# Optimization experiments

Hardware: AMD Instinct MI355X
Metric: run time of the kernel (lower is better)

The kernel has to match this reference:

```python
import jax, jax.numpy as jnp
import numpy as np
from functools import partial

C = 256
N_HEADS = 8
OFFSET_RANGE = 2.0


def _dwconv(x, w):
    # depthwise conv, SAME padding; w: (C,1,k,k)
    c = x.shape[1]
    return jax.lax.conv_general_dilated(
        x, w, window_strides=(1, 1), padding='SAME',
        feature_group_count=c, dimension_numbers=('NCHW', 'OIHW', 'NCHW'))


def _grid_sample_bilinear(x, gx, gy):
    # x: (B,C,H,W); gx,gy: (B,H,W) normalized in [-1,1]; align_corners=True
    B, Cc, H, W = x.shape
    ix = (gx + 1.0) * 0.5 * (W - 1)
    iy = (gy + 1.0) * 0.5 * (H - 1)
    x0f = jnp.floor(ix)
    y0f = jnp.floor(iy)
    fx = (ix - x0f)[:, None, :, :].reshape(B, 1, H * W)
    fy = (iy - y0f)[:, None, :, :].reshape(B, 1, H * W)
    x0 = jnp.clip(x0f.astype(jnp.int32), 0, W - 1)
    x1 = jnp.clip(x0 + 1, 0, W - 1)
    y0 = jnp.clip(y0f.astype(jnp.int32), 0, H - 1)
    y1 = jnp.clip(y0 + 1, 0, H - 1)
    xf = x.reshape(B, Cc, H * W)

    def gather(yi, xi):
        idx = (yi * W + xi).reshape(B, H * W)
        return jax.vmap(lambda f, i: f[:, i])(xf, idx)  # (B,C,N)

    v00 = gather(y0, x0)
    v01 = gather(y0, x1)
    v10 = gather(y1, x0)
    v11 = gather(y1, x1)
    out = (v00 * (1 - fx) * (1 - fy) + v01 * fx * (1 - fy)
           + v10 * (1 - fx) * fy + v11 * fx * fy)
    return out.reshape(B, Cc, H, W)


def setup_inputs() -> dict:
    key = jax.random.key(0)
    ks = jax.random.split(key, 11)
    B, H, W = 1, 64, 64
    s = 0.05
    return {
        'x': jax.random.normal(ks[0], (B, C, H, W), jnp.float32),
        'offset_weights': jnp.ones((3,), jnp.float32) + 0.1 * jax.random.normal(ks[1], (3,)),
        'w3': s * jax.random.normal(ks[2], (C, 1, 3, 3), jnp.float32),
        'w5': s * jax.random.normal(ks[3], (C, 1, 5, 5), jnp.float32),
        'w7': s * jax.random.normal(ks[4], (C, 1, 7, 7), jnp.float32),
        'w_offproj': s * jax.random.normal(ks[5], (2, C), jnp.float32),
        'wq': s * jax.random.normal(ks[6], (C, C), jnp.float32),
        'wk': s * jax.random.normal(ks[7], (C, C), jnp.float32),
        'wv': s * jax.random.normal(ks[8], (C, C), jnp.float32),
        'wo': s * jax.random.normal(ks[9], (C, C), jnp.float32),
        'beta': jnp.asarray(0.5, jnp.float32),
    }


def reference(x, offset_weights, w3, w5, w7, w_offproj, wq, wk, wv, wo, beta):
    B, Cc, H, W = x.shape
    head_dim = Cc // N_HEADS
    scale = head_dim ** -0.5
    N = H * W

    # multi-scale depthwise offset features
    off_feat = (_dwconv(x, w3) * offset_weights[0]
                + _dwconv(x, w5) * offset_weights[1]
                + _dwconv(x, w7) * offset_weights[2])
    offset = jnp.einsum('oc,bchw->bohw', w_offproj, jax.nn.relu(off_feat))  # (B,2,H,W) = (y,x)

    # reference points: ((i+0.5)/(size-1))*2 - 1
    ref_y = ((jnp.arange(H, dtype=jnp.float32) + 0.5) / (H - 1.0)) * 2.0 - 1.0
    ref_x = ((jnp.arange(W, dtype=jnp.float32) + 0.5) / (W - 1.0)) * 2.0 - 1.0
    gy = jnp.clip(ref_y[None, :, None] + jnp.tanh(offset[:, 0]) * OFFSET_RANGE, -1.0, 1.0)
    gx = jnp.clip(ref_x[None, None, :] + jnp.tanh(offset[:, 1]) * OFFSET_RANGE, -1.0, 1.0)
    x_sampled = _grid_sample_bilinear(x, gx, gy)

    # Manhattan decay bias
    yy = jnp.repeat(jnp.arange(H), W)
    xx = jnp.tile(jnp.arange(W), H)
    dist = (jnp.abs(yy[:, None] - yy[None, :]) + jnp.abs(xx[:, None] - xx[None, :])).astype(jnp.float32)
    decay = jnp.exp(-dist / (jnp.abs(beta) + 1e-6))  # (N,N)

    q = jnp.einsum('oc,bchw->bohw', wq, x).reshape(B, N_HEADS, head_dim, N)
    k = jnp.einsum('oc,bchw->bohw', wk, x_sampled).reshape(B, N_HEADS, head_dim, N)
    v = jnp.einsum('oc,bchw->bohw', wv, x_sampled).reshape(B, N_HEADS, head_dim, N)

    attn = jnp.einsum('bhdn,bhdm->bhnm', q, k) * scale + decay[None, None]
    attn = jax.nn.softmax(attn, axis=-1)
    out = jnp.einsum('bhnm,bhdm->bhdn', attn, v).reshape(B, Cc, H, W)
    return jnp.einsum('oc,bchw->bohw', wo, out)
```

## Files before the change

kernel.cpp:

```cpp
#include <hip/hip_runtime.h>
#include <hip/hip_bf16.h>


typedef __bf16 bf16x8 __attribute__((ext_vector_type(8)));
typedef float f32x4 __attribute__((ext_vector_type(4)));

__device__ __forceinline__ f32x4 mfma16(bf16x8 a, bf16x8 b, f32x4 c) {
    return __builtin_amdgcn_mfma_f32_16x16x32_bf16(a, b, c, 0, 0, 0);
}

__device__ __forceinline__ unsigned pack_bf16(float pa, float pb) {
    return __builtin_amdgcn_perm(__float_as_uint(pb), __float_as_uint(pa), 0x07060302u);
}

__global__ void transpose_kernel(const float* __restrict__ x,
                                 float* __restrict__ xTf,
                                 __hip_bfloat16* __restrict__ xTb) {
    __shared__ float tile[32][33];
    const int p0 = blockIdx.x * 32, c0 = blockIdx.y * 32;
    const int tx = threadIdx.x, ty = threadIdx.y;
#pragma unroll
    for (int i = 0; i < 4; ++i)
        tile[ty + i * 8][tx] = x[(size_t)(c0 + ty + i * 8) * 4096 + p0 + tx];
    __syncthreads();
#pragma unroll
    for (int i = 0; i < 4; ++i) {
        const float v = tile[tx][ty + i * 8];
        const size_t o = (size_t)(p0 + ty + i * 8) * 256 + c0 + tx;
        xTf[o] = v;
        xTb[o] = __float2bfloat16(v);
    }
}

__global__ void prep_kernel(const float* __restrict__ w3, const float* __restrict__ w5,
                            const float* __restrict__ w7, const float* __restrict__ ow,
                            const float* __restrict__ wq, const float* __restrict__ wk,
                            const float* __restrict__ wv, const float* __restrict__ wo,
                            float* __restrict__ wcomb, __hip_bfloat16* __restrict__ wb) {
    const int b = blockIdx.x;
    if (b < 49) {
        const int i = b, c = threadIdx.x;
        const int dy = i / 7, dx = i % 7;
        float val = ow[2] * w7[c * 49 + i];
        if (dy >= 1 && dy <= 5 && dx >= 1 && dx <= 5)
            val += ow[1] * w5[c * 25 + (dy - 1) * 5 + (dx - 1)];
        if (dy >= 2 && dy <= 4 && dx >= 2 && dx <= 4)
            val += ow[0] * w3[c * 9 + (dy - 2) * 3 + (dx - 2)];
        wcomb[i * 256 + c] = val;
    } else {
        const int idx = (b - 49) * 256 + threadIdx.x;
        const int m = idx >> 16;
        const float* src = (m == 0) ? wq : (m == 1) ? wk : (m == 2) ? wv : wo;
        const float sc = (m == 0) ? 0.25507535f : 1.0f;
        wb[idx] = __float2bfloat16(src[idx & 65535] * sc);
    }
}

__global__ __launch_bounds__(256) void sample_kernel(
    const float* __restrict__ xTf, const float* __restrict__ wcomb,
    const float* __restrict__ wop, __hip_bfloat16* __restrict__ xsT) {
    const int b = blockIdx.x;
    const int y = b >> 3;
    const int x0 = (b & 7) * 8;
    const int c = threadIdx.x;

    float wc[49];
#pragma unroll
    for (int i = 0; i < 49; ++i) wc[i] = wcomb[i * 256 + c];

    float acc[8];
#pragma unroll
    for (int px = 0; px < 8; ++px) acc[px] = 0.f;

#pragma unroll
    for (int dy = 0; dy < 7; ++dy) {
        const int yy = y + dy - 3;
        if (yy < 0 || yy > 63) continue;
        float v[14];
#pragma unroll
        for (int j = 0; j < 14; ++j) {
            const int xx = x0 - 3 + j;
            v[j] = (xx >= 0 && xx <= 63) ? xTf[(size_t)(yy * 64 + xx) * 256 + c] : 0.f;
        }
#pragma unroll
        for (int px = 0; px < 8; ++px)
#pragma unroll
            for (int dx = 0; dx < 7; ++dx)
                acc[px] = fmaf(v[px + dx], wc[dy * 7 + dx], acc[px]);
    }

    const float wy = wop[c], wx = wop[256 + c];
    float s[16];
#pragma unroll
    for (int px = 0; px < 8; ++px) {
        const float r = fmaxf(acc[px], 0.f);
        s[px] = wy * r;
        s[8 + px] = wx * r;
    }
#pragma unroll
    for (int off = 1; off < 64; off <<= 1)
#pragma unroll
        for (int i = 0; i < 16; ++i) s[i] += __shfl_xor(s[i], off, 64);

    __shared__ float red[4][16];
    const int lane = c & 63, wid = c >> 6;
    if (lane == 0)
#pragma unroll
        for (int i = 0; i < 16; ++i) red[wid][i] = s[i];
    __syncthreads();

#pragma unroll
    for (int px = 0; px < 8; ++px) {
        const float offy = red[0][px] + red[1][px] + red[2][px] + red[3][px];
        const float offx = red[0][8 + px] + red[1][8 + px] + red[2][8 + px] + red[3][8 + px];
        const int pxa = x0 + px;
        const float refy = ((y + 0.5f) / 63.0f) * 2.0f - 1.0f;
        const float refx = ((pxa + 0.5f) / 63.0f) * 2.0f - 1.0f;
        const float gy = fminf(fmaxf(refy + tanhf(offy) * 2.0f, -1.0f), 1.0f);
        const float gx = fminf(fmaxf(refx + tanhf(offx) * 2.0f, -1.0f), 1.0f);
        const float iy = (gy + 1.0f) * 31.5f;
        const float ix = (gx + 1.0f) * 31.5f;
        const float y0f = floorf(iy), x0f = floorf(ix);
        const float fy = iy - y0f, fx = ix - x0f;
        int yi0 = min(max((int)y0f, 0), 63), xi0 = min(max((int)x0f, 0), 63);
        int yi1 = min(yi0 + 1, 63), xi1 = min(xi0 + 1, 63);
        const float v00 = xTf[(size_t)(yi0 * 64 + xi0) * 256 + c];
        const float v01 = xTf[(size_t)(yi0 * 64 + xi1) * 256 + c];
        const float v10 = xTf[(size_t)(yi1 * 64 + xi0) * 256 + c];
        const float v11 = xTf[(size_t)(yi1 * 64 + xi1) * 256 + c];
        const float out = v00 * (1.f - fx) * (1.f - fy) + v01 * fx * (1.f - fy) +
                          v10 * (1.f - fx) * fy + v11 * fx * fy;
        xsT[(size_t)(y * 64 + pxa) * 256 + c] = __float2bfloat16(out);
    }
}

template <typename OutT>
__device__ __forceinline__ void gemm_body(const __hip_bfloat16* A, const __hip_bfloat16* B,
                                          OutT* out, int ldc, int m0, int n0) {
    const int w = threadIdx.x >> 6, lane = threadIdx.x & 63;
    const int g = lane >> 4, c = lane & 15;
    f32x4 acc[4];
#pragma unroll
    for (int nt = 0; nt < 4; ++nt) acc[nt] = (f32x4){0.f, 0.f, 0.f, 0.f};
    const __hip_bfloat16* Ar = A + (size_t)(m0 + w * 16 + c) * 256 + g * 8;
#pragma unroll
    for (int kc = 0; kc < 8; ++kc) {
        const bf16x8 a = *reinterpret_cast<const bf16x8*>(Ar + kc * 32);
#pragma unroll
        for (int nt = 0; nt < 4; ++nt) {
            const bf16x8 b = *reinterpret_cast<const bf16x8*>(
                B + (size_t)(n0 + nt * 16 + c) * 256 + kc * 32 + g * 8);
            acc[nt] = mfma16(a, b, acc[nt]);
        }
    }
#pragma unroll
    for (int nt = 0; nt < 4; ++nt)
#pragma unroll
        for (int r = 0; r < 4; ++r) {
            const size_t o = (size_t)(m0 + w * 16 + 4 * g + r) * ldc + n0 + nt * 16 + c;
            if constexpr (__is_same(OutT, float)) out[o] = acc[nt][r];
            else out[o] = __float2bfloat16(acc[nt][r]);
        }
}

__global__ __launch_bounds__(256) void gemm_qkv(const __hip_bfloat16* __restrict__ xq,
                                                const __hip_bfloat16* __restrict__ xs,
                                                const __hip_bfloat16* __restrict__ wb,
                                                __hip_bfloat16* __restrict__ q_t,
                                                __hip_bfloat16* __restrict__ k_t,
                                                __hip_bfloat16* __restrict__ vv) {
    const int z = blockIdx.z;
    if (z == 0)
        gemm_body<__hip_bfloat16>(xq, wb, q_t, 256, blockIdx.x * 64, blockIdx.y * 64);
    else if (z == 1)
        gemm_body<__hip_bfloat16>(xs, wb + 65536, k_t, 256, blockIdx.x * 64, blockIdx.y * 64);
    else
        gemm_body<__hip_bfloat16>(wb + 2 * 65536, xs, vv, 4096, blockIdx.y * 64,
                                  blockIdx.x * 64);
}

template <typename OutT>
__global__ __launch_bounds__(256) void gemm_abt(const __hip_bfloat16* __restrict__ A,
                                                const __hip_bfloat16* __restrict__ B,
                                                OutT* __restrict__ out, int ldc) {
    gemm_body<OutT>(A, B, out, ldc, blockIdx.x * 64, blockIdx.y * 64);
}

__global__ __launch_bounds__(256, 2) void attn_kernel(
    const __hip_bfloat16* __restrict__ q_t,
    const __hip_bfloat16* __restrict__ k_t,
    const __hip_bfloat16* __restrict__ vv,
    const float* __restrict__ beta_p,
    __hip_bfloat16* __restrict__ att)
{
    __shared__ __align__(16) char smem[34816];
    const int h = blockIdx.y;
    const int nb = blockIdx.x;
    const int n0 = nb * 64;
    const int tid = threadIdx.x;
    const int w = tid >> 6, lane = tid & 63, g = lane >> 4, c = lane & 15;

    const float bta = fabsf(beta_p[0]) + 1e-6f;
    const float L2E = 1.4426950408889634f;
    const float c2 = L2E / bta;

    float d64d[7][4];
#pragma unroll
    for (int dlt = 0; dlt < 7; ++dlt)
#pragma unroll
        for (int r = 0; r < 4; ++r) {
            const int dd = 16 * (dlt - 3) + c - 4 * g - r;
            d64d[dlt][r] = L2E * exp2f(-c2 * fabsf((float)dd));
        }

    bf16x8 aq[4];
#pragma unroll
    for (int nt = 0; nt < 4; ++nt)
        aq[nt] = *reinterpret_cast<const bf16x8*>(
            q_t + (size_t)(n0 + nt * 16 + c) * 256 + h * 32 + g * 8);

    f32x4 o_acc[4][2];
    float l_part[4] = {0.f, 0.f, 0.f, 0.f};
#pragma unroll
    for (int nt = 0; nt < 4; ++nt) {
        o_acc[nt][0] = (f32x4){0.f, 0.f, 0.f, 0.f};
        o_acc[nt][1] = (f32x4){0.f, 0.f, 0.f, 0.f};
    }

    uint2* pl = (uint2*)smem + w * 1024;
    const int wbi = g * 16 + c;
    const int rb = (g >> 1) * 64 + (g & 1) * 32 + c;
    const f32x4 zf = (f32x4){0.f, 0.f, 0.f, 0.f};

    auto loadK = [&](int it, bf16x8* bk) {
        const size_t m0 = (size_t)(it * 4 + w) * 64;
#pragma unroll
        for (int mt = 0; mt < 4; ++mt)
            bk[mt] = *reinterpret_cast<const bf16x8*>(
                k_t + (m0 + mt * 16 + c) * 256 + h * 32 + g * 8);
    };
    auto loadV = [&](int it, bf16x8 (*bv)[2]) {
        const size_t m0 = (size_t)(it * 4 + w) * 64;
#pragma unroll
        for (int dt = 0; dt < 2; ++dt)
#pragma unroll
            for (int mc = 0; mc < 2; ++mc)
                bv[dt][mc] = *reinterpret_cast<const bf16x8*>(
                    vv + (size_t)(h * 32 + dt * 16 + c) * 4096 + m0 + mc * 32 + g * 8);
    };
    auto body = [&](int it, bf16x8* bk, bf16x8 (*bv)[2]) {
        const int ym = it * 4 + w;
        const float a2 = exp2f(-c2 * fabsf((float)(nb - ym)));
#pragma unroll
        for (int nt = 0; nt < 4; ++nt) {
            f32x4 s[4];
#pragma unroll
            for (int mt = 0; mt < 4; ++mt) s[mt] = mfma16(bk[mt], aq[nt], zf);
#pragma unroll
            for (int mt = 0; mt < 4; ++mt) {
                float p[4];
#pragma unroll
                for (int r = 0; r < 4; ++r)
                    p[r] = exp2f(fmaf(a2, d64d[nt - mt + 3][r], s[mt][r]));
                l_part[nt] += (p[0] + p[1]) + (p[2] + p[3]);
                pl[wbi + (nt * 4 + mt) * 64] = uint2{pack_bf16(p[0], p[1]),
                                                     pack_bf16(p[2], p[3])};
            }
        }
#pragma unroll
        for (int nt = 0; nt < 4; ++nt)
#pragma unroll
            for (int mc = 0; mc < 2; ++mc) {
                const int idx = rb + (nt * 4 + 2 * mc) * 64;
                union { uint2 u[2]; bf16x8 v; } t;
                t.u[0] = pl[idx];
                t.u[1] = pl[idx + 16];
                o_acc[nt][0] = mfma16(t.v, bv[0][mc], o_acc[nt][0]);
                o_acc[nt][1] = mfma16(t.v, bv[1][mc], o_acc[nt][1]);
            }
    };

    bf16x8 bkA[4], bkB[4], bvA[2][2], bvB[2][2];
    loadK(0, bkA);
    loadV(0, bvA);
#pragma unroll 1
    for (int it2 = 0; it2 < 8; ++it2) {
        loadK(2 * it2 + 1, bkB);
        loadV(2 * it2 + 1, bvB);
        body(2 * it2, bkA, bvA);
        if (it2 < 7) {
            loadK(2 * it2 + 2, bkA);
            loadV(2 * it2 + 2, bvA);
        }
        body(2 * it2 + 1, bkB, bvB);
    }

#pragma unroll
    for (int nt = 0; nt < 4; ++nt) {
        float v = l_part[nt];
        v += __shfl_xor(v, 16);
        v += __shfl_xor(v, 32);
        l_part[nt] = v;
    }

    __syncthreads();
    float* ob = (float*)smem;
    float* lred = (float*)(smem + 33792);
#pragma unroll
    for (int nt = 0; nt < 4; ++nt) {
        if (g == 0) lred[w * 64 + nt * 16 + c] = l_part[nt];
#pragma unroll
        for (int r = 0; r < 4; ++r) {
            const int row = 16 * nt + 4 * g + r;
            ob[w * 2112 + row * 33 + c] = o_acc[nt][0][r];
            ob[w * 2112 + row * 33 + 16 + c] = o_acc[nt][1][r];
        }
    }
    __syncthreads();

#pragma unroll
    for (int k = 0; k < 8; ++k) {
        const int flat = k * 256 + tid;
        const int row = flat >> 5, d = flat & 31;
        const float O = ob[row * 33 + d] + ob[2112 + row * 33 + d] +
                        ob[4224 + row * 33 + d] + ob[6336 + row * 33 + d];
        const float L = lred[row] + lred[64 + row] + lred[128 + row] + lred[192 + row];
        att[(size_t)(n0 + row) * 256 + h * 32 + d] = __float2bfloat16(O / L);
    }
}

extern "C" void kernel_launch(void* const* d_in, const int* in_sizes, int n_in,
                              void* d_out, int out_size, void* d_ws, size_t ws_size,
                              hipStream_t stream) {
    (void)in_sizes; (void)n_in; (void)out_size; (void)ws_size;
    const float* x    = (const float*)d_in[0];
    const float* ow   = (const float*)d_in[1];
    const float* w3   = (const float*)d_in[2];
    const float* w5   = (const float*)d_in[3];
    const float* w7   = (const float*)d_in[4];
    const float* wop  = (const float*)d_in[5];
    const float* wq   = (const float*)d_in[6];
    const float* wk   = (const float*)d_in[7];
    const float* wv   = (const float*)d_in[8];
    const float* wo   = (const float*)d_in[9];
    const float* beta = (const float*)d_in[10];

    char* ws = (char*)d_ws;
    const size_t MB = 1 << 20;
    float*          xTf = (float*)(ws);
    __hip_bfloat16* xTb = (__hip_bfloat16*)(ws + 4 * MB);
    __hip_bfloat16* xsT = (__hip_bfloat16*)(ws + 6 * MB);
    __hip_bfloat16* q_t = (__hip_bfloat16*)(ws + 8 * MB);
    __hip_bfloat16* k_t = (__hip_bfloat16*)(ws + 10 * MB);
    __hip_bfloat16* vv  = (__hip_bfloat16*)(ws + 12 * MB);
    __hip_bfloat16* att = (__hip_bfloat16*)(ws + 14 * MB);
    __hip_bfloat16* wb  = (__hip_bfloat16*)(ws + 16 * MB);
    float* wcomb        = (float*)(ws + 16 * MB + 512 * 1024);
    __hip_bfloat16* wob = wb + 3 * 65536;

    transpose_kernel<<<dim3(128, 8), dim3(32, 8), 0, stream>>>(x, xTf, xTb);
    prep_kernel<<<1073, 256, 0, stream>>>(w3, w5, w7, ow, wq, wk, wv, wo, wcomb, wb);
    sample_kernel<<<512, 256, 0, stream>>>(xTf, wcomb, wop, xsT);
    gemm_qkv<<<dim3(64, 4, 3), 256, 0, stream>>>(xTb, xsT, wb, q_t, k_t, vv);
    attn_kernel<<<dim3(64, 8), 256, 0, stream>>>(q_t, k_t, vv, beta, att);
    gemm_abt<float><<<dim3(4, 64), 256, 0, stream>>>(wob, att, (float*)d_out, 4096);
}
```

Baseline: 163.7 us.

## Halve attention query tile to 32 rows and double grid for occupancy

The attention kernel now processes 32 query rows per block instead of 64 and launches twice as many blocks (1024 instead of 512), so the work spreads better across the many CUs. Registers and shared memory shrink, so launch bounds are raised to 4 blocks per CU. V loads are no longer double-buffered but issued inside the body, and the output reduction buffer stride is changed to 36. The cost is that each K/V tile is now reloaded by twice as many blocks, and V load latency is less hidden.

Measured after the change: 206.4 us. +26.1%, slower.

```diff
diff --git a/kernel.cpp b/kernel.cpp
--- a/kernel.cpp
+++ b/kernel.cpp
@@ -186,17 +186,19 @@
     gemm_body<OutT>(A, B, out, ldc, blockIdx.x * 64, blockIdx.y * 64);
 }
 
-__global__ __launch_bounds__(256, 2) void attn_kernel(
+__global__ __launch_bounds__(256, 4) void attn_kernel(
     const __hip_bfloat16* __restrict__ q_t,
     const __hip_bfloat16* __restrict__ k_t,
     const __hip_bfloat16* __restrict__ vv,
     const float* __restrict__ beta_p,
     __hip_bfloat16* __restrict__ att)
 {
-    __shared__ __align__(16) char smem[34816];
+    __shared__ __align__(16) char smem[18944];
     const int h = blockIdx.y;
-    const int nb = blockIdx.x;
-    const int n0 = nb * 64;
+    const int nb2 = blockIdx.x;
+    const int n0 = nb2 * 32;
+    const int yq = nb2 >> 1;
+    const int half = nb2 & 1;
     const int tid = threadIdx.x;
     const int w = tid >> 6, lane = tid & 63, g = lane >> 4, c = lane & 15;
 
@@ -204,30 +206,30 @@
     const float L2E = 1.4426950408889634f;
     const float c2 = L2E / bta;
 
-    float d64d[7][4];
-#pragma unroll
-    for (int dlt = 0; dlt < 7; ++dlt)
+    float d64d[5][4];
+#pragma unroll
+    for (int dlt = 0; dlt < 5; ++dlt)
 #pragma unroll
         for (int r = 0; r < 4; ++r) {
-            const int dd = 16 * (dlt - 3) + c - 4 * g - r;
+            const int dd = 16 * (dlt - 3) + 32 * half + c - 4 * g - r;
             d64d[dlt][r] = L2E * exp2f(-c2 * fabsf((float)dd));
         }
 
-    bf16x8 aq[4];
-#pragma unroll
-    for (int nt = 0; nt < 4; ++nt)
+    bf16x8 aq[2];
+#pragma unroll
+    for (int nt = 0; nt < 2; ++nt)
         aq[nt] = *reinterpret_cast<const bf16x8*>(
             q_t + (size_t)(n0 + nt * 16 + c) * 256 + h * 32 + g * 8);
 
-    f32x4 o_acc[4][2];
-    float l_part[4] = {0.f, 0.f, 0.f, 0.f};
-#pragma unroll
-    for (int nt = 0; nt < 4; ++nt) {
+    f32x4 o_acc[2][2];
+    float l_part[2] = {0.f, 0.f};
+#pragma unroll
+    for (int nt = 0; nt < 2; ++nt) {
         o_acc[nt][0] = (f32x4){0.f, 0.f, 0.f, 0.f};
         o_acc[nt][1] = (f32x4){0.f, 0.f, 0.f, 0.f};
     }
 
-    uint2* pl = (uint2*)smem + w * 1024;
+    uint2* pl = (uint2*)smem + w * 512;
     const int wbi = g * 16 + c;
     const int rb = (g >> 1) * 64 + (g & 1) * 32 + c;
     const f32x4 zf = (f32x4){0.f, 0.f, 0.f, 0.f};
@@ -239,20 +241,20 @@
             bk[mt] = *reinterpret_cast<const bf16x8*>(
                 k_t + (m0 + mt * 16 + c) * 256 + h * 32 + g * 8);
     };
-    auto loadV = [&](int it, bf16x8 (*bv)[2]) {
-        const size_t m0 = (size_t)(it * 4 + w) * 64;
+    auto body = [&](int it, bf16x8* bk) {
+        const int ym = it * 4 + w;
+        const size_t m0 = (size_t)ym * 64;
+        bf16x8 bv[2][2];
 #pragma unroll
         for (int dt = 0; dt < 2; ++dt)
 #pragma unroll
             for (int mc = 0; mc < 2; ++mc)
                 bv[dt][mc] = *reinterpret_cast<const bf16x8*>(
                     vv + (size_t)(h * 32 + dt * 16 + c) * 4096 + m0 + mc * 32 + g * 8);
-    };
-    auto body = [&](int it, bf16x8* bk, bf16x8 (*bv)[2]) {
-        const int ym = it * 4 + w;
-        const float a2 = exp2f(-c2 * fabsf((float)(nb - ym)));
-#pragma unroll
-        for (int nt = 0; nt < 4; ++nt) {
+
+        const float a2 = exp2f(-c2 * fabsf((float)(yq - ym)));
+#pragma unroll
+        for (int nt = 0; nt < 2; ++nt) {
             f32x4 s[4];
 #pragma unroll
             for (int mt = 0; mt < 4; ++mt) s[mt] = mfma16(bk[mt], aq[nt], zf);
@@ -268,7 +270,7 @@
             }
         }
 #pragma unroll
-        for (int nt = 0; nt < 4; ++nt)
+        for (int nt = 0; nt < 2; ++nt)
 #pragma unroll
             for (int mc = 0; mc < 2; ++mc) {
                 const int idx = rb + (nt * 4 + 2 * mc) * 64;
@@ -280,23 +282,18 @@
             }
     };
 
-    bf16x8 bkA[4], bkB[4], bvA[2][2], bvB[2][2];
+    bf16x8 bkA[4], bkB[4];
     loadK(0, bkA);
-    loadV(0, bvA);
 #pragma unroll 1
     for (int it2 = 0; it2 < 8; ++it2) {
         loadK(2 * it2 + 1, bkB);
-        loadV(2 * it2 + 1, bvB);
-        body(2 * it2, bkA, bvA);
-        if (it2 < 7) {
-            loadK(2 * it2 + 2, bkA);
-            loadV(2 * it2 + 2, bvA);
-        }
-        body(2 * it2 + 1, bkB, bvB);
-    }
-
-#pragma unroll
-    for (int nt = 0; nt < 4; ++nt) {
+        body(2 * it2, bkA);
+        if (it2 < 7) loadK(2 * it2 + 2, bkA);
+        body(2 * it2 + 1, bkB);
+    }
+
+#pragma unroll
+    for (int nt = 0; nt < 2; ++nt) {
         float v = l_part[nt];
         v += __shfl_xor(v, 16);
         v += __shfl_xor(v, 32);
@@ -305,26 +302,26 @@
 
     __syncthreads();
     float* ob = (float*)smem;
-    float* lred = (float*)(smem + 33792);
-#pragma unroll
-    for (int nt = 0; nt < 4; ++nt) {
-        if (g == 0) lred[w * 64 + nt * 16 + c] = l_part[nt];
+    float* lred = (float*)(smem + 18432);
+#pragma unroll
+    for (int nt = 0; nt < 2; ++nt) {
+        if (g == 0) lred[w * 32 + nt * 16 + c] = l_part[nt];
 #pragma unroll
         for (int r = 0; r < 4; ++r) {
             const int row = 16 * nt + 4 * g + r;
-            ob[w * 2112 + row * 33 + c] = o_acc[nt][0][r];
-            ob[w * 2112 + row * 33 + 16 + c] = o_acc[nt][1][r];
+            ob[w * 1152 + row * 36 + c] = o_acc[nt][0][r];
+            ob[w * 1152 + row * 36 + 16 + c] = o_acc[nt][1][r];
         }
     }
     __syncthreads();
 
 #pragma unroll
-    for (int k = 0; k < 8; ++k) {
+    for (int k = 0; k < 4; ++k) {
         const int flat = k * 256 + tid;
         const int row = flat >> 5, d = flat & 31;
-        const float O = ob[row * 33 + d] + ob[2112 + row * 33 + d] +
-                        ob[4224 + row * 33 + d] + ob[6336 + row * 33 + d];
-        const float L = lred[row] + lred[64 + row] + lred[128 + row] + lred[192 + row];
+        const float O = ob[row * 36 + d] + ob[1152 + row * 36 + d] +
+                        ob[2304 + row * 36 + d] + ob[3456 + row * 36 + d];
+        const float L = lred[row] + lred[32 + row] + lred[64 + row] + lred[96 + row];
         att[(size_t)(n0 + row) * 256 + h * 32 + d] = __float2bfloat16(O / L);
     }
 }
@@ -362,6 +359,6 @@
     prep_kernel<<<1073, 256, 0, stream>>>(w3, w5, w7, ow, wq, wk, wv, wo, wcomb, wb);
     sample_kernel<<<512, 256, 0, stream>>>(xTf, wcomb, wop, xsT);
     gemm_qkv<<<dim3(64, 4, 3), 256, 0, stream>>>(xTb, xsT, wb, q_t, k_t, vv);
-    attn_kernel<<<dim3(64, 8), 256, 0, stream>>>(q_t, k_t, vv, beta, att);
+    attn_kernel<<<dim3(128, 8), 256, 0, stream>>>(q_t, k_t, vv, beta, att);
     gemm_abt<float><<<dim3(4, 64), 256, 0, stream>>>(wob, att, (float*)d_out, 4096);
 }
```
